# Kernel tuning notes

Hardware: AMD Instinct MI355X
Metric: run time of the kernel (lower is better)

## Reference

```python
import jax, jax.numpy as jnp
import numpy as np

D_MODEL = 2048
N_HEADS = 16
HEAD_DIM = D_MODEL // N_HEADS
D_FF = 8192


def setup_inputs() -> dict:
    key = jax.random.key(0)
    ks = jax.random.split(key, 16)
    s = 0.02
    inp = {
        'x': jax.random.normal(ks[0], (2, 2048, D_MODEL), dtype=jnp.float32),
        'Wq': jax.random.normal(ks[1], (D_MODEL, D_MODEL), jnp.float32) * s,
        'bq': jnp.zeros((D_MODEL,), jnp.float32),
        'Wk': jax.random.normal(ks[2], (D_MODEL, D_MODEL), jnp.float32) * s,
        'bk': jnp.zeros((D_MODEL,), jnp.float32),
        'Wv': jax.random.normal(ks[3], (D_MODEL, D_MODEL), jnp.float32) * s,
        'bv': jnp.zeros((D_MODEL,), jnp.float32),
        'Wo': jax.random.normal(ks[4], (D_MODEL, D_MODEL), jnp.float32) * s,
        'bo': jnp.zeros((D_MODEL,), jnp.float32),
        'rotary': jax.random.normal(ks[5], (1, 1, HEAD_DIM), jnp.float32) * s,
        'norm1_w': jnp.ones((D_MODEL,), jnp.float32),
        'norm2_w': jnp.ones((D_MODEL,), jnp.float32),
        'W1': jax.random.normal(ks[6], (2 * D_FF, D_MODEL), jnp.float32) * s,
        'b1': jnp.zeros((2 * D_FF,), jnp.float32),
        'W2': jax.random.normal(ks[7], (D_MODEL, D_FF), jnp.float32) * s,
        'b2': jnp.zeros((D_MODEL,), jnp.float32),
    }
    return inp


def _rmsnorm(x, w, eps=1e-8):
    return w * (x * jax.lax.rsqrt(jnp.mean(x * x, axis=-1, keepdims=True) + eps))


def reference(x, Wq, bq, Wk, bk, Wv, bv, Wo, bo, rotary, norm1_w, norm2_w, W1, b1, W2, b2):
    B, S, _ = x.shape
    # --- attention block ---
    h = _rmsnorm(x, norm1_w)
    q = (h @ Wq.T + bq).reshape(B, S, N_HEADS, HEAD_DIM)
    k = (h @ Wk.T + bk).reshape(B, S, N_HEADS, HEAD_DIM)
    v = (h @ Wv.T + bv).reshape(B, S, N_HEADS, HEAD_DIM)
    q = q + rotary  # (1,1,head_dim) broadcast over batch, seq, heads
    scores = jnp.einsum('bqhd,bkhd->bhqk', q, k) / jnp.sqrt(jnp.float32(HEAD_DIM))
    attn = jax.nn.softmax(scores, axis=-1)
    o = jnp.einsum('bhqk,bkhd->bqhd', attn, v).reshape(B, S, D_MODEL)
    x = x + (o @ Wo.T + bo)
    # --- SwiGLU FFN block ---
    h2 = _rmsnorm(x, norm2_w)
    g = h2 @ W1.T + b1
    x1, x2 = g[..., :D_FF], g[..., D_FF:]
    ff = (x1 * jax.nn.silu(x2)) @ W2.T + b2
    return x + ff
```

## Files before the change

### kernel.cpp

```cpp
#include <hip/hip_runtime.h>
#include <hip/hip_bf16.h>

#define D_MODEL 2048
#define N_HEADS 16
#define HEAD_DIM 128
#define D_FF 8192
#define BATCH 2
#define SEQ 2048
#define M_TOK (BATCH * SEQ)
#define QKV_LD 6144
#define QSCALE 0.12751744f

typedef __attribute__((ext_vector_type(8))) short short8;
typedef __attribute__((ext_vector_type(4))) short short4v;
typedef __attribute__((ext_vector_type(4))) float f32x4;
typedef __attribute__((ext_vector_type(16))) float f32x16;
typedef __attribute__((ext_vector_type(2))) unsigned int uint2v;
typedef __attribute__((ext_vector_type(4))) unsigned int uint4v;

__device__ __forceinline__ unsigned short f2b(float f) {
  __hip_bfloat16 h = __float2bfloat16(f);
  return *reinterpret_cast<unsigned short*>(&h);
}
__device__ __forceinline__ float b2f(unsigned short u) {
  unsigned int x = ((unsigned int)u) << 16;
  return __uint_as_float(x);
}

__device__ __forceinline__ void gload_lds16(const void* gsrc, void* ldst) {
  __builtin_amdgcn_global_load_lds(
      (const __attribute__((address_space(1))) void*)gsrc,
      (__attribute__((address_space(3))) void*)ldst, 16, 0, 0);
}

__device__ __forceinline__ f32x16 mfma32(short8 a, short8 b, f32x16 c) {
  return __builtin_amdgcn_mfma_f32_32x32x16_bf16(a, b, c, 0, 0, 0);
}
__device__ __forceinline__ unsigned int cvtpk(float lo, float hi) {
  unsigned int r;
  asm("v_cvt_pk_bf16_f32 %0, %1, %2" : "=v"(r) : "v"(lo), "v"(hi));
  return r;
}
__device__ __forceinline__ uint2v plswap(unsigned int a, unsigned int b) {
  return __builtin_amdgcn_permlane32_swap(a, b, false, false);
}

__global__ __launch_bounds__(256)
void cvt_kernel(const float* __restrict__ src, unsigned short* __restrict__ dst,
                int nchunks, float scale) {
  int i = blockIdx.x * blockDim.x + threadIdx.x;
  int stride = gridDim.x * blockDim.x;
  for (int c = i; c < nchunks; c += stride) {
    const float4 a = *(const float4*)(src + (size_t)c * 8);
    const float4 b = *(const float4*)(src + (size_t)c * 8 + 4);
    short8 r;
    r[0] = f2b(a.x * scale); r[1] = f2b(a.y * scale);
    r[2] = f2b(a.z * scale); r[3] = f2b(a.w * scale);
    r[4] = f2b(b.x * scale); r[5] = f2b(b.y * scale);
    r[6] = f2b(b.z * scale); r[7] = f2b(b.w * scale);
    *(short8*)(dst + (size_t)c * 8) = r;
  }
}

__global__ __launch_bounds__(256)
void cvt_w1p_kernel(const float* __restrict__ src,
                    unsigned short* __restrict__ dst) {
  int i = blockIdx.x * blockDim.x + threadIdx.x;
  int stride = gridDim.x * blockDim.x;
  const int total = 2 * D_FF * (D_MODEL / 8);
  for (int c = i; c < total; c += stride) {
    int rp = c >> 8, col8 = c & 255;
    int b = rp >> 6, half = (rp >> 5) & 1;
    int rs = half * D_FF + b * 32 + (rp & 31);
    const float* s = src + (size_t)rs * D_MODEL + col8 * 8;
    const float4 a = *(const float4*)s;
    const float4 bb = *(const float4*)(s + 4);
    short8 r;
    r[0] = f2b(a.x); r[1] = f2b(a.y); r[2] = f2b(a.z); r[3] = f2b(a.w);
    r[4] = f2b(bb.x); r[5] = f2b(bb.y); r[6] = f2b(bb.z); r[7] = f2b(bb.w);
    *(short8*)(dst + (size_t)c * 8) = r;
  }
}

__global__ void permb1_kernel(const float* __restrict__ b1,
                              float* __restrict__ b1p) {
  int i = blockIdx.x * 256 + threadIdx.x;
  int b = i >> 6, half = (i >> 5) & 1;
  b1p[i] = b1[half * D_FF + b * 32 + (i & 31)];
}

__global__ void biasqkv_kernel(const float* __restrict__ bq,
                               const float* __restrict__ bk,
                               const float* __restrict__ bv,
                               const float* __restrict__ rot,
                               float* __restrict__ outp) {
  int i = blockIdx.x * 256 + threadIdx.x;
  float v;
  if (i < 2048) v = (bq[i] + rot[i & (HEAD_DIM - 1)]) * QSCALE;
  else if (i < 4096) v = bk[i - 2048];
  else v = bv[i - 4096];
  outp[i] = v;
}

__global__ __launch_bounds__(256)
void rmsnorm_kernel(const float* __restrict__ x, const float* __restrict__ wv,
                    unsigned short* __restrict__ outp) {
  const int row = blockIdx.x;
  const float* xr = x + (size_t)row * D_MODEL;
  const int base = threadIdx.x * 8;
  float4 a = *(const float4*)(xr + base);
  float4 c = *(const float4*)(xr + base + 4);
  float ss = a.x * a.x + a.y * a.y + a.z * a.z + a.w * a.w +
             c.x * c.x + c.y * c.y + c.z * c.z + c.w * c.w;
#pragma unroll
  for (int m = 1; m < 64; m <<= 1) ss += __shfl_xor(ss, m);
  __shared__ float red[4];
  if ((threadIdx.x & 63) == 0) red[threadIdx.x >> 6] = ss;
  __syncthreads();
  float tot = red[0] + red[1] + red[2] + red[3];
  float sc = rsqrtf(tot * (1.0f / D_MODEL) + 1e-8f);
  float4 w0 = *(const float4*)(wv + base);
  float4 w1 = *(const float4*)(wv + base + 4);
  short8 r;
  r[0] = f2b(a.x * sc * w0.x); r[1] = f2b(a.y * sc * w0.y);
  r[2] = f2b(a.z * sc * w0.z); r[3] = f2b(a.w * sc * w0.w);
  r[4] = f2b(c.x * sc * w1.x); r[5] = f2b(c.y * sc * w1.y);
  r[6] = f2b(c.z * sc * w1.z); r[7] = f2b(c.w * sc * w1.w);
  *(short8*)(outp + (size_t)row * D_MODEL + base) = r;
}

template <int MODE>
__global__ __launch_bounds__(512, 2)
void gemm_p8(const unsigned short* __restrict__ A, int lda,
             const unsigned short* __restrict__ W, int ldw,
             const float* __restrict__ bias, void* __restrict__ outp,
             int N, int K, size_t out_zstride) {
  __shared__ unsigned short AL[2][2][128 * 64];
  __shared__ unsigned short BL[2][2][128 * 64];
  const int t = threadIdx.x;
  const int l = t & 63, w = t >> 6;
  const int wm = w >> 2, wn = w & 3;
  const int ln = l & 31, hi = l >> 5;
  const int m0 = blockIdx.y << 8, n0 = blockIdx.x << 8;
  const int koff = blockIdx.z * K;

  const int r0 = t >> 3;
  const int cb16 = (t & 7) * 16;
  const int sel = ((cb16 ^ ((r0 & 7) << 4)) >> 1);
  const unsigned short* Abase = A + (size_t)m0 * lda + koff;
  const unsigned short* Wbase = W + (size_t)n0 * ldw + koff;
  const int d0e = t * 8, d1e = (t + 512) * 8;

#define STAGE(XL, Xb, ld, dd, h, ktd)                                        \
  do {                                                                       \
    const unsigned short* s_ =                                               \
        (Xb) + (size_t)((h) * 128 + r0) * (ld) + (ktd) * 64 + sel;           \
    gload_lds16(s_, &XL[dd][h][d0e]);                                        \
    gload_lds16(s_ + (size_t)64 * (ld), &XL[dd][h][d1e]);                    \
  } while (0)

  const int swz = (ln & 7) << 4;
  const int hb = wn >> 1;
  const int browb = ((wn & 1) * 64 + ln) * 128;

  f32x16 acc[4][2] = {};
  short8 bf[2][4];

#define READB(dd)                                                            \
  do {                                                                       \
    const char* Bb_ = (const char*)&BL[dd][hb][0];                           \
    _Pragma("unroll") for (int cb_ = 0; cb_ < 2; cb_++)                      \
      _Pragma("unroll") for (int ks_ = 0; ks_ < 4; ks_++)                    \
        bf[cb_][ks_] = *(const short8*)(Bb_ + browb + cb_ * 4096 +           \
                                        ((ks_ * 32 + hi * 16) ^ swz));       \
  } while (0)

#define PHASE2(dd, p, STAGE_STMT, VM_STMT)                                   \
  do {                                                                       \
    const char* Ab_ = (const char*)&AL[dd][p][0];                            \
    short8 af_[2][4];                                                        \
    if ((p) == 0) READB(dd);                                                 \
    _Pragma("unroll") for (int sb_ = 0; sb_ < 2; sb_++) {                    \
      _Pragma("unroll") for (int ks_ = 0; ks_ < 4; ks_++)                    \
        af_[sb_][ks_] = *(const short8*)(Ab_ +                               \
                                         (wm * 64 + sb_ * 32 + ln) * 128 +   \
                                         ((ks_ * 32 + hi * 16) ^ swz));      \
    }                                                                        \
    STAGE_STMT;                                                              \
    __builtin_amdgcn_sched_barrier(0);                                       \
    VM_STMT;                                                                 \
    __builtin_amdgcn_sched_barrier(0);                                       \
    __builtin_amdgcn_s_barrier();                                            \
    __builtin_amdgcn_sched_barrier(0);                                       \
    __builtin_amdgcn_s_setprio(1);                                           \
    _Pragma("unroll") for (int sb_ = 0; sb_ < 2; sb_++)                      \
      _Pragma("unroll") for (int cb_ = 0; cb_ < 2; cb_++)                    \
        _Pragma("unroll") for (int ks_ = 0; ks_ < 4; ks_++)                  \
          acc[2 * (p) + sb_][cb_] =                                          \
              mfma32(af_[sb_][ks_], bf[cb_][ks_], acc[2 * (p) + sb_][cb_]);  \
    __builtin_amdgcn_s_setprio(0);                                           \
    __builtin_amdgcn_sched_barrier(0);                                       \
    __builtin_amdgcn_s_barrier();                                            \
    __builtin_amdgcn_sched_barrier(0);                                       \
  } while (0)

  const int NT = K >> 6;

  STAGE(AL, Abase, lda, 0, 0, 0);
  STAGE(AL, Abase, lda, 0, 1, 0);
  STAGE(BL, Wbase, ldw, 0, 0, 0);
  STAGE(BL, Wbase, ldw, 0, 1, 0);
  STAGE(AL, Abase, lda, 1, 0, 1);
  STAGE(BL, Wbase, ldw, 1, 0, 1);
  asm volatile("s_waitcnt vmcnt(4)" ::: "memory");
  __builtin_amdgcn_sched_barrier(0);
  __builtin_amdgcn_s_barrier();
  __builtin_amdgcn_sched_barrier(0);

  for (int kt = 0; kt < NT; kt += 2) {
    PHASE2(0, 0,
           {
             if (kt + 1 < NT) {
               STAGE(BL, Wbase, ldw, 1, 1, kt + 1);
               STAGE(AL, Abase, lda, 1, 1, kt + 1);
             }
           },
           {});
    PHASE2(0, 1,
           {
             if (kt + 2 < NT) {
               STAGE(AL, Abase, lda, 0, 0, kt + 2);
               STAGE(BL, Wbase, ldw, 0, 0, kt + 2);
             }
           },
           {
             if (kt + 2 < NT)
               asm volatile("s_waitcnt vmcnt(4)" ::: "memory");
             else
               asm volatile("s_waitcnt vmcnt(0)" ::: "memory");
           });
    PHASE2(1, 0,
           {
             if (kt + 2 < NT) {
               STAGE(BL, Wbase, ldw, 0, 1, kt + 2);
               STAGE(AL, Abase, lda, 0, 1, kt + 2);
             }
           },
           {});
    PHASE2(1, 1,
           {
             if (kt + 3 < NT) {
               STAGE(AL, Abase, lda, 1, 0, kt + 3);
               STAGE(BL, Wbase, ldw, 1, 0, kt + 3);
             }
           },
           {
             if (kt + 3 < NT)
               asm volatile("s_waitcnt vmcnt(4)" ::: "memory");
             else
               asm volatile("s_waitcnt vmcnt(0)" ::: "memory");
           });
  }
#undef PHASE2
#undef READB
#undef STAGE

#pragma unroll
  for (int rb = 0; rb < 4; rb++) {
    const int rowb = m0 + (rb >> 1) * 128 + wm * 64 + (rb & 1) * 32 + 4 * hi;
    if (MODE == 3) {
      const int col0 = n0 + wn * 64 + ln;
      const float b1v = bias[col0];
      const float b2v = bias[col0 + 32];
      const int jout = (n0 >> 1) + wn * 32 + ln;
#pragma unroll
      for (int r = 0; r < 16; r++) {
        const int row = rowb + (r & 3) + 8 * (r >> 2);
        float x1 = acc[rb][0][r] + b1v;
        float x2 = acc[rb][1][r] + b2v;
        float sg = x2 / (1.0f + __expf(-x2));
        ((unsigned short*)outp)[(size_t)row * (N >> 1) + jout] = f2b(x1 * sg);
      }
    } else {
#pragma unroll
      for (int cb = 0; cb < 2; cb++) {
        const int col = n0 + wn * 64 + cb * 32 + ln;
        const float bv = (MODE == 0) ? bias[col] : 0.0f;
#pragma unroll
        for (int r = 0; r < 16; r++) {
          const int row = rowb + (r & 3) + 8 * (r >> 2);
          const float vv = acc[rb][cb][r] + bv;
          if (MODE == 0)
            ((unsigned short*)outp)[(size_t)row * N + col] = f2b(vv);
          else
            ((float*)outp + blockIdx.z * out_zstride)[(size_t)row * N + col] = vv;
        }
      }
    }
  }
}

template <int MODE>
__global__ __launch_bounds__(256)
void gemm_bt(const unsigned short* __restrict__ A, int lda,
             const unsigned short* __restrict__ W, int ldw,
             const float* __restrict__ bias, const float* res, void* outp,
             int N, int K, size_t out_zstride) {
  __shared__ unsigned short As[128 * 32];
  __shared__ unsigned short Bs[128 * 32];
  const int t = threadIdx.x;
  const int l = t & 63;
  const int w = t >> 6;
  const int m0 = blockIdx.y << 7;
  const int n0 = blockIdx.x << 7;
  const int wr = (w >> 1) << 6;
  const int wc = (w & 1) << 6;
  const int koff = blockIdx.z * K;

  const unsigned short* Ab = A + (size_t)m0 * lda + koff;
  const unsigned short* Wb = W + (size_t)n0 * ldw + koff;

  f32x4 acc[4][4] = {};

  const int c0 = t, c1 = t + 256;
  const int ar0 = c0 >> 2, ak0 = (c0 & 3) * 8;
  const int ar1 = c1 >> 2, ak1 = (c1 & 3) * 8;
  const int lr = l & 15, lk = (l >> 4) * 8;

  for (int k0 = 0; k0 < K; k0 += 32) {
    gload_lds16(Ab + (size_t)ar0 * lda + k0 + ak0, &As[c0 * 8]);
    gload_lds16(Ab + (size_t)ar1 * lda + k0 + ak1, &As[c1 * 8]);
    gload_lds16(Wb + (size_t)ar0 * ldw + k0 + ak0, &Bs[c0 * 8]);
    gload_lds16(Wb + (size_t)ar1 * ldw + k0 + ak1, &Bs[c1 * 8]);
    __syncthreads();
    short8 a[4], b[4];
#pragma unroll
    for (int mi = 0; mi < 4; mi++)
      a[mi] = *(const short8*)&As[(wr + mi * 16 + lr) * 32 + lk];
#pragma unroll
    for (int ni = 0; ni < 4; ni++)
      b[ni] = *(const short8*)&Bs[(wc + ni * 16 + lr) * 32 + lk];
#pragma unroll
    for (int mi = 0; mi < 4; mi++)
#pragma unroll
      for (int ni = 0; ni < 4; ni++)
        acc[mi][ni] = __builtin_amdgcn_mfma_f32_16x16x32_bf16(
            a[mi], b[ni], acc[mi][ni], 0, 0, 0);
    __syncthreads();
  }

  const int lg = (l >> 4) * 4;
#pragma unroll
  for (int mi = 0; mi < 4; mi++) {
#pragma unroll
    for (int ni = 0; ni < 4; ni++) {
      int cn = n0 + wc + ni * 16 + lr;
      float bval = bias[cn];
#pragma unroll
      for (int j = 0; j < 4; j++) {
        int r = m0 + wr + mi * 16 + lg + j;
        float vv = acc[mi][ni][j] + bval;
        size_t idx = (size_t)r * N + cn;
        ((float*)outp)[idx] = vv + res[idx];
      }
    }
  }
  (void)out_zstride;
}

__global__ __launch_bounds__(256)
void vtrans_kernel(const unsigned short* __restrict__ qkv,
                   unsigned short* __restrict__ vt) {
  const int bh = blockIdx.y;
  const int b = bh >> 4, h = bh & 15;
  const int s0 = blockIdx.x * 32;
  __shared__ unsigned short tile[32][136];
  const int t = threadIdx.x;
  for (int i = 0; i < 2; i++) {
    int c = t + i * 256;
    int s = c >> 4, dc = c & 15;
    *(short8*)&tile[s][dc * 8] =
        *(const short8*)(qkv + (size_t)(b * SEQ + s0 + s) * QKV_LD + 4096 +
                         h * HEAD_DIM + dc * 8);
  }
  __syncthreads();
  const int d = t >> 1, sh = (t & 1) * 16;
  unsigned short* dst = vt + ((size_t)bh * HEAD_DIM + d) * SEQ + s0 + sh;
  short8 r0, r1;
#pragma unroll
  for (int j = 0; j < 8; j++) r0[j] = tile[sh + j][d];
#pragma unroll
  for (int j = 0; j < 8; j++) r1[j] = tile[sh + 8 + j][d];
  *(short8*)dst = r0;
  *(short8*)(dst + 8) = r1;
}

__global__ __launch_bounds__(512, 2)
void attn_kernel(const unsigned short* __restrict__ qkv,
                 const unsigned short* __restrict__ vt,
                 unsigned short* __restrict__ o) {
  const int bh = blockIdx.y;
  const int b = bh >> 4, h = bh & 15;
  const int q0 = blockIdx.x << 8;
  const int t = threadIdx.x, w = t >> 6, l = t & 63;
  const int ln = l & 31, hi = l >> 5;

  __shared__ unsigned short Ks[2][64 * 128];

  short8 qf[8];
  {
    const unsigned short* qb =
        qkv + (size_t)(b * SEQ + q0 + w * 32 + ln) * QKV_LD + h * HEAD_DIM +
        hi * 8;
#pragma unroll
    for (int sl = 0; sl < 8; sl++) qf[sl] = *(const short8*)(qb + sl * 16);
  }

  f32x16 oacc[4] = {};
  float mrow = -1e30f, lrow = 0.f;

  const unsigned short* kbase =
      qkv + (size_t)(b * SEQ) * QKV_LD + 2048 + h * HEAD_DIM;
  const unsigned short* vbase = vt + (size_t)bh * HEAD_DIM * SEQ;

#define STAGEK(buf, kv0_)                                                    \
  do {                                                                       \
    _Pragma("unroll") for (int i_ = 0; i_ < 2; i_++) {                       \
      int c_ = t + i_ * 512;                                                 \
      int row_ = c_ >> 4, dc_ = c_ & 15;                                     \
      int sel_ = ((dc_ * 16) ^ ((row_ & 7) << 4)) >> 1;                      \
      gload_lds16(kbase + (size_t)((kv0_) + row_) * QKV_LD + sel_,           \
                  &Ks[buf][c_ * 8]);                                         \
    }                                                                        \
  } while (0)

  STAGEK(0, 0);
  __syncthreads();

  for (int it = 0; it < SEQ / 64; ++it) {
    const int cur = it & 1;
    const int kv0 = it * 64;

    short8 vf[4][4];
#pragma unroll
    for (int db = 0; db < 4; db++)
#pragma unroll
      for (int ks = 0; ks < 4; ks++)
        vf[db][ks] = *(const short8*)(vbase + (size_t)(db * 32 + ln) * SEQ +
                                      kv0 + ks * 16 + hi * 8);

    if (it + 1 < SEQ / 64) STAGEK(cur ^ 1, kv0 + 64);

    const char* kb = (const char*)&Ks[cur][0];
    f32x16 s0 = {}, s1 = {};
#pragma unroll
    for (int sl = 0; sl < 8; sl++) {
      const int cw = (sl * 32 + hi * 16) ^ ((ln & 7) << 4);
      short8 kf0 = *(const short8*)(kb + ln * 256 + cw);
      short8 kf1 = *(const short8*)(kb + (32 + ln) * 256 + cw);
      s0 = mfma32(kf0, qf[sl], s0);
      s1 = mfma32(kf1, qf[sl], s1);
    }

    float mx = s0[0];
#pragma unroll
    for (int r = 1; r < 16; r++) mx = fmaxf(mx, s0[r]);
#pragma unroll
    for (int r = 0; r < 16; r++) mx = fmaxf(mx, s1[r]);
    {
      uint2v r2 = plswap(__float_as_uint(mx), __float_as_uint(mx));
      mx = fmaxf(__uint_as_float(r2[0]), __uint_as_float(r2[1]));
    }

    if (!__all(mx <= mrow + 8.f)) {
      float mnew = fmaxf(mrow, mx);
      float fs = exp2f(mrow - mnew);
      mrow = mnew;
      lrow *= fs;
#pragma unroll
      for (int db = 0; db < 4; db++)
#pragma unroll
        for (int r = 0; r < 16; r++) oacc[db][r] *= fs;
    }

    float p0[16], p1[16];
    float sum = 0.f;
#pragma unroll
    for (int r = 0; r < 16; r++) {
      p0[r] = exp2f(s0[r] - mrow);
      sum += p0[r];
    }
#pragma unroll
    for (int r = 0; r < 16; r++) {
      p1[r] = exp2f(s1[r] - mrow);
      sum += p1[r];
    }
    lrow += sum;

    uint4v pk[4];
#define PACKSUB(P, K0)                                                       \
  {                                                                          \
    unsigned int a_, b_;                                                     \
    uint2v r_;                                                               \
    a_ = cvtpk(P[0], P[1]); b_ = cvtpk(P[4], P[5]);                          \
    r_ = plswap(a_, b_); pk[K0][0] = r_[0]; pk[K0][2] = r_[1];               \
    a_ = cvtpk(P[2], P[3]); b_ = cvtpk(P[6], P[7]);                          \
    r_ = plswap(a_, b_); pk[K0][1] = r_[0]; pk[K0][3] = r_[1];               \
    a_ = cvtpk(P[8], P[9]); b_ = cvtpk(P[12], P[13]);                        \
    r_ = plswap(a_, b_); pk[K0 + 1][0] = r_[0]; pk[K0 + 1][2] = r_[1];       \
    a_ = cvtpk(P[10], P[11]); b_ = cvtpk(P[14], P[15]);                      \
    r_ = plswap(a_, b_); pk[K0 + 1][1] = r_[0]; pk[K0 + 1][3] = r_[1];       \
  }
    PACKSUB(p0, 0);
    PACKSUB(p1, 2);
#undef PACKSUB

#pragma unroll
    for (int db = 0; db < 4; db++)
#pragma unroll
      for (int ks = 0; ks < 4; ks++)
        oacc[db] = mfma32(vf[db][ks], __builtin_bit_cast(short8, pk[ks]),
                          oacc[db]);

    __syncthreads();
  }
#undef STAGEK

  {
    uint2v r2 = plswap(__float_as_uint(lrow), __float_as_uint(lrow));
    lrow = __uint_as_float(r2[0]) + __uint_as_float(r2[1]);
  }
  const float inv = 1.0f / lrow;
  unsigned short* ob = o + (size_t)(b * SEQ + q0 + w * 32 + ln) * D_MODEL +
                       h * HEAD_DIM + hi * 4;
#pragma unroll
  for (int db = 0; db < 4; db++)
#pragma unroll
    for (int r = 0; r < 4; r++) {
      short4v v4;
#pragma unroll
      for (int j = 0; j < 4; j++)
        v4[j] = (short)f2b(oacc[db][4 * r + j] * inv);
      *(short4v*)(ob + db * 32 + r * 8) = v4;
    }
}

__global__ __launch_bounds__(256)
void reduce2_kernel(const float* __restrict__ p0, const float* __restrict__ p1,
                    const float* __restrict__ b2, float* __restrict__ out) {
  size_t i = (size_t)blockIdx.x * 256 + threadIdx.x;
  float4 a = ((const float4*)p0)[i];
  float4 b = ((const float4*)p1)[i];
  float4 o = ((const float4*)out)[i];
  float4 bb = ((const float4*)b2)[i & 511];
  o.x += a.x + b.x + bb.x;
  o.y += a.y + b.y + bb.y;
  o.z += a.z + b.z + bb.z;
  o.w += a.w + b.w + bb.w;
  ((float4*)out)[i] = o;
}

extern "C" void kernel_launch(void* const* d_in, const int* in_sizes, int n_in,
                              void* d_out, int out_size, void* d_ws,
                              size_t ws_size, hipStream_t stream) {
  (void)in_sizes; (void)n_in; (void)out_size; (void)ws_size;
  const float* x   = (const float*)d_in[0];
  const float* Wq  = (const float*)d_in[1];
  const float* bq  = (const float*)d_in[2];
  const float* Wk  = (const float*)d_in[3];
  const float* bk  = (const float*)d_in[4];
  const float* Wv  = (const float*)d_in[5];
  const float* bv  = (const float*)d_in[6];
  const float* Wo  = (const float*)d_in[7];
  const float* bo  = (const float*)d_in[8];
  const float* rot = (const float*)d_in[9];
  const float* n1w = (const float*)d_in[10];
  const float* n2w = (const float*)d_in[11];
  const float* W1  = (const float*)d_in[12];
  const float* b1  = (const float*)d_in[13];
  const float* W2  = (const float*)d_in[14];
  const float* b2  = (const float*)d_in[15];
  float* out = (float*)d_out;
  char* ws = (char*)d_ws;

  const size_t SZ_D2  = (size_t)D_MODEL * D_MODEL * 2;
  const size_t SZ_ACT = (size_t)M_TOK * D_MODEL * 2;
  const size_t SZ_W1  = (size_t)2 * D_FF * D_MODEL * 2;
  const size_t SZ_W2  = (size_t)D_MODEL * D_FF * 2;
  const size_t SZ_G   = (size_t)M_TOK * 2 * D_FF * 2;

  size_t off = 0;
  auto alloc = [&](size_t sz) { size_t o = off; off += (sz + 255) & ~(size_t)255; return o; };
  unsigned short* wqkv_b = (unsigned short*)(ws + alloc(3 * SZ_D2));
  unsigned short* wo_b   = (unsigned short*)(ws + alloc(SZ_D2));
  unsigned short* w1_b   = (unsigned short*)(ws + alloc(SZ_W1));
  unsigned short* w2_b   = (unsigned short*)(ws + alloc(SZ_W2));
  float*          biasq  = (float*)(ws + alloc(QKV_LD * 4));
  float*          b1p    = (float*)(ws + alloc(2 * D_FF * 4));
  unsigned short* h2_b   = (unsigned short*)(ws + alloc(SZ_ACT));
  char* pool = ws + alloc(SZ_G);
  unsigned short* h_b   = (unsigned short*)(pool);
  unsigned short* qkv_b = (unsigned short*)(pool + SZ_ACT);
  unsigned short* vt_b  = (unsigned short*)(pool + 4 * SZ_ACT);
  unsigned short* o_b   = (unsigned short*)(pool + 5 * SZ_ACT);
  unsigned short* ff_b  = (unsigned short*)(pool);
  float* p0 = (float*)ws;
  float* p1 = p0 + (size_t)M_TOK * D_MODEL;

  cvt_kernel<<<1024, 256, 0, stream>>>(Wq, wqkv_b, D_MODEL * D_MODEL / 8, QSCALE);
  cvt_kernel<<<1024, 256, 0, stream>>>(Wk, wqkv_b + (size_t)D_MODEL * D_MODEL, D_MODEL * D_MODEL / 8, 1.0f);
  cvt_kernel<<<1024, 256, 0, stream>>>(Wv, wqkv_b + (size_t)2 * D_MODEL * D_MODEL, D_MODEL * D_MODEL / 8, 1.0f);
  cvt_kernel<<<1024, 256, 0, stream>>>(Wo, wo_b, D_MODEL * D_MODEL / 8, 1.0f);
  cvt_w1p_kernel<<<2048, 256, 0, stream>>>(W1, w1_b);
  cvt_kernel<<<2048, 256, 0, stream>>>(W2, w2_b, D_MODEL * D_FF / 8, 1.0f);
  biasqkv_kernel<<<QKV_LD / 256, 256, 0, stream>>>(bq, bk, bv, rot, biasq);
  permb1_kernel<<<2 * D_FF / 256, 256, 0, stream>>>(b1, b1p);

  rmsnorm_kernel<<<M_TOK, 256, 0, stream>>>(x, n1w, h_b);

  gemm_p8<0><<<dim3(QKV_LD / 256, M_TOK / 256), 512, 0, stream>>>(
      h_b, D_MODEL, wqkv_b, D_MODEL, biasq, qkv_b, QKV_LD, D_MODEL, 0);

  vtrans_kernel<<<dim3(SEQ / 32, BATCH * N_HEADS), 256, 0, stream>>>(qkv_b, vt_b);
  attn_kernel<<<dim3(SEQ / 256, BATCH * N_HEADS), 512, 0, stream>>>(qkv_b, vt_b, o_b);

  gemm_bt<1><<<dim3(D_MODEL / 128, M_TOK / 128), 256, 0, stream>>>(
      o_b, D_MODEL, wo_b, D_MODEL, bo, x, out, D_MODEL, D_MODEL, 0);

  rmsnorm_kernel<<<M_TOK, 256, 0, stream>>>(out, n2w, h2_b);

  gemm_p8<3><<<dim3(2 * D_FF / 256, M_TOK / 256), 512, 0, stream>>>(
      h2_b, D_MODEL, w1_b, D_MODEL, b1p, ff_b, 2 * D_FF, D_MODEL, 0);

  gemm_p8<2><<<dim3(D_MODEL / 256, M_TOK / 256, 2), 512, 0, stream>>>(
      ff_b, D_FF, w2_b, D_FF, nullptr, p0, D_MODEL, D_FF / 2,
      (size_t)M_TOK * D_MODEL);

  reduce2_kernel<<<(M_TOK * D_MODEL / 4) / 256, 256, 0, stream>>>(p0, p1, b2, out);
}
```

Baseline: 915.4 us.

## Route output projection through split-K 256-tile GEMM, add setprio in attention

The Wo projection moves off the simple 128x128 single-buffered GEMM and onto the pipelined 256x256 gemm_p8 kernel with split-K of 2, writing fp32 partials that a new elementwise kernel sums with bias and residual. The attention kernel raises wave priority around its MFMA sections, and the SwiGLU epilogue uses a hardware reciprocal instead of a division. The split-K path adds an extra round trip of two fp32 partial buffers through memory, traded against better MFMA utilisation in the GEMM.

```diff
diff --git a/kernel.cpp b/kernel.cpp
--- a/kernel.cpp
+++ b/kernel.cpp
@@ -278,7 +278,7 @@
         const int row = rowb + (r & 3) + 8 * (r >> 2);
         float x1 = acc[rb][0][r] + b1v;
         float x2 = acc[rb][1][r] + b2v;
-        float sg = x2 / (1.0f + __expf(-x2));
+        float sg = x2 * __builtin_amdgcn_rcpf(1.0f + __expf(-x2));
         ((unsigned short*)outp)[(size_t)row * (N >> 1) + jout] = f2b(x1 * sg);
       }
     } else {
@@ -298,74 +298,6 @@
       }
     }
   }
-}
-
-template <int MODE>
-__global__ __launch_bounds__(256)
-void gemm_bt(const unsigned short* __restrict__ A, int lda,
-             const unsigned short* __restrict__ W, int ldw,
-             const float* __restrict__ bias, const float* res, void* outp,
-             int N, int K, size_t out_zstride) {
-  __shared__ unsigned short As[128 * 32];
-  __shared__ unsigned short Bs[128 * 32];
-  const int t = threadIdx.x;
-  const int l = t & 63;
-  const int w = t >> 6;
-  const int m0 = blockIdx.y << 7;
-  const int n0 = blockIdx.x << 7;
-  const int wr = (w >> 1) << 6;
-  const int wc = (w & 1) << 6;
-  const int koff = blockIdx.z * K;
-
-  const unsigned short* Ab = A + (size_t)m0 * lda + koff;
-  const unsigned short* Wb = W + (size_t)n0 * ldw + koff;
-
-  f32x4 acc[4][4] = {};
-
-  const int c0 = t, c1 = t + 256;
-  const int ar0 = c0 >> 2, ak0 = (c0 & 3) * 8;
-  const int ar1 = c1 >> 2, ak1 = (c1 & 3) * 8;
-  const int lr = l & 15, lk = (l >> 4) * 8;
-
-  for (int k0 = 0; k0 < K; k0 += 32) {
-    gload_lds16(Ab + (size_t)ar0 * lda + k0 + ak0, &As[c0 * 8]);
-    gload_lds16(Ab + (size_t)ar1 * lda + k0 + ak1, &As[c1 * 8]);
-    gload_lds16(Wb + (size_t)ar0 * ldw + k0 + ak0, &Bs[c0 * 8]);
-    gload_lds16(Wb + (size_t)ar1 * ldw + k0 + ak1, &Bs[c1 * 8]);
-    __syncthreads();
-    short8 a[4], b[4];
-#pragma unroll
-    for (int mi = 0; mi < 4; mi++)
-      a[mi] = *(const short8*)&As[(wr + mi * 16 + lr) * 32 + lk];
-#pragma unroll
-    for (int ni = 0; ni < 4; ni++)
-      b[ni] = *(const short8*)&Bs[(wc + ni * 16 + lr) * 32 + lk];
-#pragma unroll
-    for (int mi = 0; mi < 4; mi++)
-#pragma unroll
-      for (int ni = 0; ni < 4; ni++)
-        acc[mi][ni] = __builtin_amdgcn_mfma_f32_16x16x32_bf16(
-            a[mi], b[ni], acc[mi][ni], 0, 0, 0);
-    __syncthreads();
-  }
-
-  const int lg = (l >> 4) * 4;
-#pragma unroll
-  for (int mi = 0; mi < 4; mi++) {
-#pragma unroll
-    for (int ni = 0; ni < 4; ni++) {
-      int cn = n0 + wc + ni * 16 + lr;
-      float bval = bias[cn];
-#pragma unroll
-      for (int j = 0; j < 4; j++) {
-        int r = m0 + wr + mi * 16 + lg + j;
-        float vv = acc[mi][ni][j] + bval;
-        size_t idx = (size_t)r * N + cn;
-        ((float*)outp)[idx] = vv + res[idx];
-      }
-    }
-  }
-  (void)out_zstride;
 }
 
 __global__ __launch_bounds__(256)
@@ -453,6 +385,7 @@
 
     const char* kb = (const char*)&Ks[cur][0];
     f32x16 s0 = {}, s1 = {};
+    __builtin_amdgcn_s_setprio(1);
 #pragma unroll
     for (int sl = 0; sl < 8; sl++) {
       const int cw = (sl * 32 + hi * 16) ^ ((ln & 7) << 4);
@@ -461,6 +394,7 @@
       s0 = mfma32(kf0, qf[sl], s0);
       s1 = mfma32(kf1, qf[sl], s1);
     }
+    __builtin_amdgcn_s_setprio(0);
 
     float mx = s0[0];
 #pragma unroll
@@ -515,12 +449,14 @@
     PACKSUB(p1, 2);
 #undef PACKSUB
 
+    __builtin_amdgcn_s_setprio(1);
 #pragma unroll
     for (int db = 0; db < 4; db++)
 #pragma unroll
       for (int ks = 0; ks < 4; ks++)
         oacc[db] = mfma32(vf[db][ks], __builtin_bit_cast(short8, pk[ks]),
                           oacc[db]);
+    __builtin_amdgcn_s_setprio(0);
 
     __syncthreads();
   }
@@ -543,6 +479,23 @@
         v4[j] = (short)f2b(oacc[db][4 * r + j] * inv);
       *(short4v*)(ob + db * 32 + r * 8) = v4;
     }
+}
+
+__global__ __launch_bounds__(256)
+void reduceo_kernel(const float* __restrict__ p0, const float* __restrict__ p1,
+                    const float* __restrict__ bo, const float* __restrict__ x,
+                    float* __restrict__ out) {
+  size_t i = (size_t)blockIdx.x * 256 + threadIdx.x;
+  float4 a = ((const float4*)p0)[i];
+  float4 b = ((const float4*)p1)[i];
+  float4 xx = ((const float4*)x)[i];
+  float4 bb = ((const float4*)bo)[i & 511];
+  float4 o;
+  o.x = a.x + b.x + xx.x + bb.x;
+  o.y = a.y + b.y + xx.y + bb.y;
+  o.z = a.z + b.z + xx.z + bb.z;
+  o.w = a.w + b.w + xx.w + bb.w;
+  ((float4*)out)[i] = o;
 }
 
 __global__ __launch_bounds__(256)
@@ -603,6 +556,8 @@
   unsigned short* qkv_b = (unsigned short*)(pool + SZ_ACT);
   unsigned short* vt_b  = (unsigned short*)(pool + 4 * SZ_ACT);
   unsigned short* o_b   = (unsigned short*)(pool + 5 * SZ_ACT);
+  float* po0 = (float*)pool;
+  float* po1 = po0 + (size_t)M_TOK * D_MODEL;
   unsigned short* ff_b  = (unsigned short*)(pool);
   float* p0 = (float*)ws;
   float* p1 = p0 + (size_t)M_TOK * D_MODEL;
@@ -624,8 +579,11 @@
   vtrans_kernel<<<dim3(SEQ / 32, BATCH * N_HEADS), 256, 0, stream>>>(qkv_b, vt_b);
   attn_kernel<<<dim3(SEQ / 256, BATCH * N_HEADS), 512, 0, stream>>>(qkv_b, vt_b, o_b);
 
-  gemm_bt<1><<<dim3(D_MODEL / 128, M_TOK / 128), 256, 0, stream>>>(
-      o_b, D_MODEL, wo_b, D_MODEL, bo, x, out, D_MODEL, D_MODEL, 0);
+  gemm_p8<2><<<dim3(D_MODEL / 256, M_TOK / 256, 2), 512, 0, stream>>>(
+      o_b, D_MODEL, wo_b, D_MODEL, nullptr, po0, D_MODEL, D_MODEL / 2,
+      (size_t)M_TOK * D_MODEL);
+  reduceo_kernel<<<(M_TOK * D_MODEL / 4) / 256, 256, 0, stream>>>(
+      po0, po1, bo, x, out);
 
   rmsnorm_kernel<<<M_TOK, 256, 0, stream>>>(out, n2w, h2_b);
 
```

Result: faster. 877.8 us (-4.1%).
